# Optimization experiments

Measured on AMD Instinct MI355X. Metric: run time of the kernel, lower is better.

## Reference

```python
import jax, jax.numpy as jnp
import numpy as np

EPS = float(np.finfo(np.float32).eps)
NUM_SAMPLES = 2000
Y0 = 0.9999
BATCH, ACTION_DIM = 4096, 16


def setup_inputs() -> dict:
    key = jax.random.key(0)
    k1, k2, k3 = jax.random.split(key, 3)
    mean = jax.random.normal(k1, (BATCH, ACTION_DIM), dtype=jnp.float32)
    std = jax.random.uniform(k2, (BATCH, ACTION_DIM), dtype=jnp.float32)
    uniform = jax.random.uniform(k3, (BATCH, ACTION_DIM, 1), dtype=jnp.float32)
    return {"mean": mean, "std": std, "uniform": uniform}


def reference(mean, std, uniform):
    # Matches CustomDistribution.__init__ (std + eps) and rsample().
    std = std + EPS                                     # (B, A)
    grid = jnp.linspace(-Y0, Y0, NUM_SAMPLES, dtype=jnp.float32)  # (S,)
    x = grid[None, None, :]                             # broadcast to (1, 1, S)
    mu = mean[..., None]                                # (B, A, 1)
    sg = std[..., None]                                 # (B, A, 1)

    atanh_x = 0.5 * jnp.log((1.0 + x) / (1.0 - x) + EPS)
    log_term = (atanh_x - mu) ** 2 / (-2.0 * sg ** 2)
    # unnormalized density of tanh-Gaussian on the grid: (B, A, S)
    probs = (1.0 / (1.0 - x ** 2)) * (1.0 / jnp.sqrt(2.0 * jnp.pi * sg ** 2)) * jnp.exp(log_term)
    probs = probs / (probs.sum(axis=2, keepdims=True) + EPS)

    cdf = jnp.cumsum(probs, axis=2)                     # (B, A, S)
    # first index where uniform < cdf (argmax of bool picks first True)
    sample_idx = jnp.argmax(uniform < cdf, axis=2)      # (B, A) int

    sampled_values = grid[sample_idx]                   # (B, A)
    sampled_probs = jnp.take_along_axis(probs, sample_idx[..., None], axis=2)[..., 0]
    return sampled_values, sampled_probs
```

## Files before the change

kernel.cpp:

```cpp
#include <hip/hip_runtime.h>
#include <math.h>

#define NS 2000
#define NPAD 2048
#define EPS_F 1.1920928955078125e-07f
#define LOG2E 1.4426950408889634f
#define X0F  -0.9999f
#define HREC 999.64996f
#define HF   1.00040020e-3f
#define B8C  2.7842747f
#define SIGM 2.0e-3f
#define PCELL_MIN 1.0e-4f
#define FLIP_TOL 0.012f

__device__ __forceinline__ float exp2_hw(float x) {
    return __builtin_amdgcn_exp2f(x);
}

template <int CTRL, int RMASK>
static __device__ __forceinline__ float dpp_add(float x) {
    int t = __builtin_amdgcn_update_dpp(0, __float_as_int(x), CTRL, RMASK, 0xf, true);
    return x + __int_as_float(t);
}
static __device__ __forceinline__ float scan64(float x) {
    x = dpp_add<0x111, 0xf>(x);
    x = dpp_add<0x112, 0xf>(x);
    x = dpp_add<0x114, 0xf>(x);
    x = dpp_add<0x118, 0xf>(x);
    x = dpp_add<0x142, 0xa>(x);
    x = dpp_add<0x143, 0xc>(x);
    return x;
}
static __device__ __forceinline__ float scan32(float x) {
    x = dpp_add<0x111, 0xf>(x);
    x = dpp_add<0x112, 0xf>(x);
    x = dpp_add<0x114, 0xf>(x);
    x = dpp_add<0x118, 0xf>(x);
    x = dpp_add<0x142, 0xa>(x);
    return x;
}
static __device__ __forceinline__ float bcast_lane(float x, int lane_sgpr) {
    return __int_as_float(__builtin_amdgcn_readlane(__float_as_int(x), lane_sgpr));
}

static __device__ __forceinline__ float cdf01(float t) {
    float z = -t * 0.70710678f;
    float az = fabsf(z);
    float k = 1.0f / fmaf(0.3275911f, az, 1.0f);
    float poly = fmaf(k, 1.061405429f, -1.453152027f);
    poly = fmaf(k, poly, 1.421413741f);
    poly = fmaf(k, poly, -0.284496736f);
    poly = fmaf(k, poly, 0.254829592f);
    poly *= k;
    float e = exp2_hw(-az * az * LOG2E);
    float erfc_az = poly * e;
    float erfc_z = (z < 0.0f) ? (2.0f - erfc_az) : erfc_az;
    return 0.5f * erfc_z;
}
static __device__ __forceinline__ float erfinv_f(float x) {
    float w = -logf(fmaf(-x, x, 1.0f));
    bool c = w < 5.0f;
    float ww = c ? (w - 2.5f) : (sqrtf(w) - 3.0f);
    float p = c ? 2.81022636e-08f : -0.000200214257f;
    p = fmaf(p, ww, c ? 3.43273939e-07f : 0.000100950558f);
    p = fmaf(p, ww, c ? -3.5233877e-06f : 0.00134934322f);
    p = fmaf(p, ww, c ? -4.39150654e-06f : -0.00367342844f);
    p = fmaf(p, ww, c ? 0.00021858087f : 0.00573950773f);
    p = fmaf(p, ww, c ? -0.00125372503f : -0.0076224613f);
    p = fmaf(p, ww, c ? -0.00417768164f : 0.00943887047f);
    p = fmaf(p, ww, c ? 0.246640727f : 1.00167406f);
    p = fmaf(p, ww, c ? 1.50140941f : 2.83297682f);
    return p * x;
}
static __device__ __forceinline__ float cosh2f(float t) {
    float e = exp2_hw(2.8853901f * t);
    float re = __builtin_amdgcn_rcpf(e);
    return 0.25f * (e + 2.0f + re);
}

__global__ void build_table(float2* __restrict__ tabT, float2* __restrict__ tab2,
                            int* __restrict__ cnt) {
    int i = blockIdx.x * blockDim.x + threadIdx.x;
    if (i == 0) *cnt = 0;
    if (i >= NPAD) return;
    float a = 0.0f, lw = -1000.0f;
    if (i < NS) {
        const double y0 = -0.9999, y1 = 0.9999;
        const double step = (y1 - y0) / 1999.0;
        float x = (i == NS - 1) ? (float)y1 : (float)(y0 + (double)i * step);
        float ratio = (1.0f + x) / (1.0f - x) + EPS_F;
        a = 0.5f * logf(ratio);
        float w = 1.0f / (1.0f - x * x);
        lw = log2f(w);
    }
    tab2[i] = make_float2(a, lw);
    int l = i >> 5, k = i & 31, kk = k >> 1, h = k & 1;
    tabT[(kk * 64 + l) * 2 + h] = make_float2(a, lw);
}

__global__ __launch_bounds__(256) void analytic_kernel(
    const float* __restrict__ mean, const float* __restrict__ stdv,
    const float* __restrict__ uni, const float2* __restrict__ tab2,
    float* __restrict__ out_vals, float* __restrict__ out_probs,
    int* __restrict__ list, int* __restrict__ cnt, int nElem) {
    int gid = blockIdx.x * blockDim.x + threadIdx.x;
    if (gid >= nElem) return;

    const float mu = mean[gid];
    const float sg = stdv[gid] + EPS_F;
    const float u = uni[gid];
    const float inv_sg = 1.0f / sg;
    const float rd2 = -0.72134752f * inv_sg * inv_sg;
    const float nc = 0.39894228f * inv_sg;
    const float hn = HF * nc;

    float ql[8];
    float qlow = 0.0f, qhigh = 0.0f;
    #pragma unroll
    for (int c = 0; c < 8; c++) {
        float2 al = tab2[c];
        float d = al.x - mu;
        ql[c] = exp2_hw(fmaf(d * d, rd2, al.y));
        qlow += ql[c];
        float2 ah = tab2[NS - 8 + c];
        float dh = ah.x - mu;
        qhigh += exp2_hw(fmaf(dh * dh, rd2, ah.y));
    }

    const float PloB = cdf01((-B8C - mu) * inv_sg);
    const float PhiB = cdf01(( B8C - mu) * inv_sg);
    const float Qbulk = fmaxf(PhiB - PloB, 0.0f) / hn;
    const float Stot = qlow + Qbulk + qhigh;
    const float denomP = fmaf(nc, Stot, EPS_F);
    const float tt = u * denomP / nc;

    bool ok = (sg >= SIGM * cosh2f(fminf(fabsf(mu), B8C)));
    ok = ok && (tt < qlow + Qbulk);

    int idx = -1;
    float qsel = 0.0f;

    {
        float cum = 0.0f;
        #pragma unroll
        for (int c = 0; c < 8; c++) {
            cum += ql[c];
            if (idx < 0 && cum > tt) { idx = c; qsel = ql[c]; }
        }
    }
    if (ok && idx < 0) {
        float Pt = fmaf(tt - qlow, hn, PloB);
        float xx = fmaf(2.0f, Pt, -1.0f);
        xx = fminf(fmaxf(xx, -0.99999994f), 0.99999994f);
        float ts = 1.41421356f * erfinv_f(xx);
        float as = fmaf(sg, ts, mu);
        float e2 = exp2_hw(as * 2.8853901f);
        float tau = 1.0f - 2.0f / (e2 + 1.0f);
        float fi = fmaf(tau - X0F, HREC, -0.5f);
        int is = (int)floorf(fi) + 1;
        ok = ok && (is >= 8) && (is <= 1991)
                && (sg >= SIGM * cosh2f(fabsf(as)));
        is = min(max(is, 8), 1991);
        float2 al = tab2[is];
        float d = al.x - mu;
        float qi = exp2_hw(fmaf(d * d, rd2, al.y));
        float pn = nc * qi / denomP;
        ok = ok && (pn >= PCELL_MIN);
        float hl = HF * cosh2f(fabsf(as));
        float r = hl * inv_sg;
        float arg = r * (fabsf(as - mu) * inv_sg + 0.5f * r);
        float ratio = exp2_hw(LOG2E * fminf(arg, 20.0f)) - 1.0f;
        ok = ok && (pn * ratio <= FLIP_TOL);
        if (ok) { idx = is; qsel = qi; }
    }

    if (ok && idx >= 0) {
        const double y0 = -0.9999, y1 = 0.9999;
        const double step = (y1 - y0) / 1999.0;
        float gv = (idx == NS - 1) ? (float)y1 : (float)(y0 + (double)idx * step);
        out_vals[gid] = gv;
        out_probs[gid] = nc * qsel / denomP;
    } else {
        int slot = atomicAdd(cnt, 1);
        list[slot] = gid;
    }
}

__global__ __launch_bounds__(256) void fallback_kernel(
    const float* __restrict__ mean, const float* __restrict__ stdv,
    const float* __restrict__ uni, const float4* __restrict__ gT,
    const float4* __restrict__ gP,
    float* __restrict__ out_vals, float* __restrict__ out_probs,
    const int* __restrict__ list, const int* __restrict__ cnt) {
    const int count = *cnt;
    if (blockIdx.x * 4 >= count) return;

    __shared__ float4 sT[NPAD / 2];
    __shared__ float4 sPbuf[NPAD / 2];
    const float2* sP = (const float2*)sPbuf;
    for (int t = threadIdx.x; t < NPAD / 2; t += 256) {
        sT[t] = gT[t];
        sPbuf[t] = gP[t];
    }
    __syncthreads();

    const int lane = threadIdx.x & 63;
    const int wid = threadIdx.x >> 6;
    const int stride = gridDim.x << 2;

    for (int slot = blockIdx.x * 4 + wid; slot < count; slot += stride) {
        const int elem = list[slot];
        const float mu = mean[elem];
        const float sg = stdv[elem] + EPS_F;
        const float u = uni[elem];
        const float sg2 = sg * sg;
        const float rden2 = LOG2E / (-2.0f * sg2);
        const float normc = 1.0f / sqrtf(6.2831853071795864f * sg2);

        float s0 = 0.0f, s1 = 0.0f;
        #pragma unroll
        for (int kk = 0; kk < 16; kk++) {
            float4 v = sT[kk * 64 + lane];
            float d0 = v.x - mu;
            s0 += exp2_hw(fmaf(d0 * d0, rden2, v.y));
            float d1 = v.z - mu;
            s1 += exp2_hw(fmaf(d1 * d1, rden2, v.w));
        }
        float s = s0 + s1;

        float incl = scan64(s);
        const float S = bcast_lane(incl, 63);
        const float denom = S * normc + EPS_F;
        const float tt = (u * denom) / normc;

        unsigned long long mgt = __ballot(incl > tt);
        int jstar = mgt ? __builtin_ctzll(mgt) : 64;
        int jj = (jstar < 64) ? jstar : 0;
        float exclb = bcast_lane(incl - s, jj);

        int c = lane & 31;
        float2 al = sP[jj * 32 + c];
        float d = al.x - mu;
        float cum = scan32(exp2_hw(fmaf(d * d, rden2, al.y)));
        cum += exclb;
        unsigned int m2 = (unsigned int)(__ballot(cum > tt) & 0xffffffffULL);
        int sub = m2 ? (int)__builtin_ctz(m2) : 32;
        int idx = (jstar >= 64) ? 0 : min(jj * 32 + sub, NS - 1);

        if (lane == 0) {
            float2 al2 = sP[idx];
            float dd = al2.x - mu;
            float pk = exp2_hw(fmaf(dd * dd, rden2, al2.y)) * normc;
            const double y0 = -0.9999, y1 = 0.9999;
            const double step = (y1 - y0) / 1999.0;
            float gv = (idx == NS - 1) ? (float)y1
                                       : (float)(y0 + (double)idx * step);
            out_vals[elem] = gv;
            out_probs[elem] = pk / denom;
        }
    }
}

extern "C" void kernel_launch(void* const* d_in, const int* in_sizes, int n_in,
                              void* d_out, int out_size, void* d_ws, size_t ws_size,
                              hipStream_t stream) {
    const float* mean = (const float*)d_in[0];
    const float* stdv = (const float*)d_in[1];
    const float* uni = (const float*)d_in[2];
    float* out = (float*)d_out;
    const int nElem = in_sizes[0];
    float* out_vals = out;
    float* out_probs = out + nElem;

    char* ws = (char*)d_ws;
    float2* tabT = (float2*)ws;
    float2* tab2 = (float2*)(ws + 16384);
    int* cnt = (int*)(ws + 32768);
    int* list = (int*)(ws + 32768 + 16);

    build_table<<<NPAD / 256, 256, 0, stream>>>(tabT, tab2, cnt);

    analytic_kernel<<<(nElem + 255) / 256, 256, 0, stream>>>(
        mean, stdv, uni, tab2, out_vals, out_probs, list, cnt, nElem);

    fallback_kernel<<<2048, 256, 0, stream>>>(
        mean, stdv, uni, (const float4*)tabT, (const float4*)tab2,
        out_vals, out_probs, list, cnt);
}
```

Baseline: 75.65 us.

## Fuse table build, analytic sampling and fallback into one kernel

Replaces the three-kernel pipeline (table build, analytic fast path, global-list fallback) with a single kernel. Each block does the analytic path for its elements, collects failures in a shared-memory list, and only when that list is non-empty rebuilds the grid tables in LDS and runs the brute-force fallback for those elements. This removes two launches, the global atomic counter and list, and the global table round-trip. In exchange, table values are recomputed per element on the fast path (log/div per lookup), and every block with any fallback rebuilds the full table in LDS. Fallback work is also confined to its own block rather than spread across 2048 blocks.

```diff
diff --git a/kernel.cpp b/kernel.cpp
--- a/kernel.cpp
+++ b/kernel.cpp
@@ -12,6 +12,7 @@
 #define SIGM 2.0e-3f
 #define PCELL_MIN 1.0e-4f
 #define FLIP_TOL 0.012f
+#define BLOCK 256
 
 __device__ __forceinline__ float exp2_hw(float x) {
     return __builtin_amdgcn_exp2f(x);
@@ -78,138 +79,135 @@
     return 0.25f * (e + 2.0f + re);
 }
 
-__global__ void build_table(float2* __restrict__ tabT, float2* __restrict__ tab2,
-                            int* __restrict__ cnt) {
-    int i = blockIdx.x * blockDim.x + threadIdx.x;
-    if (i == 0) *cnt = 0;
-    if (i >= NPAD) return;
-    float a = 0.0f, lw = -1000.0f;
-    if (i < NS) {
-        const double y0 = -0.9999, y1 = 0.9999;
-        const double step = (y1 - y0) / 1999.0;
-        float x = (i == NS - 1) ? (float)y1 : (float)(y0 + (double)i * step);
-        float ratio = (1.0f + x) / (1.0f - x) + EPS_F;
-        a = 0.5f * logf(ratio);
-        float w = 1.0f / (1.0f - x * x);
-        lw = log2f(w);
-    }
-    tab2[i] = make_float2(a, lw);
-    int l = i >> 5, k = i & 31, kk = k >> 1, h = k & 1;
-    tabT[(kk * 64 + l) * 2 + h] = make_float2(a, lw);
-}
-
-__global__ __launch_bounds__(256) void analytic_kernel(
+static __device__ __forceinline__ float2 cellAL(int i) {
+    const double y0 = -0.9999, y1 = 0.9999;
+    const double step = (y1 - y0) / 1999.0;
+    float x = (i == NS - 1) ? (float)y1 : (float)(y0 + (double)i * step);
+    float ratio = (1.0f + x) / (1.0f - x) + EPS_F;
+    float a = 0.5f * logf(ratio);
+    float lw = log2f(1.0f / (1.0f - x * x));
+    return make_float2(a, lw);
+}
+
+__global__ __launch_bounds__(BLOCK) void fused_kernel(
     const float* __restrict__ mean, const float* __restrict__ stdv,
-    const float* __restrict__ uni, const float2* __restrict__ tab2,
-    float* __restrict__ out_vals, float* __restrict__ out_probs,
-    int* __restrict__ list, int* __restrict__ cnt, int nElem) {
-    int gid = blockIdx.x * blockDim.x + threadIdx.x;
-    if (gid >= nElem) return;
-
-    const float mu = mean[gid];
-    const float sg = stdv[gid] + EPS_F;
-    const float u = uni[gid];
-    const float inv_sg = 1.0f / sg;
-    const float rd2 = -0.72134752f * inv_sg * inv_sg;
-    const float nc = 0.39894228f * inv_sg;
-    const float hn = HF * nc;
-
-    float ql[8];
-    float qlow = 0.0f, qhigh = 0.0f;
-    #pragma unroll
-    for (int c = 0; c < 8; c++) {
-        float2 al = tab2[c];
-        float d = al.x - mu;
-        ql[c] = exp2_hw(fmaf(d * d, rd2, al.y));
-        qlow += ql[c];
-        float2 ah = tab2[NS - 8 + c];
-        float dh = ah.x - mu;
-        qhigh += exp2_hw(fmaf(dh * dh, rd2, ah.y));
-    }
-
-    const float PloB = cdf01((-B8C - mu) * inv_sg);
-    const float PhiB = cdf01(( B8C - mu) * inv_sg);
-    const float Qbulk = fmaxf(PhiB - PloB, 0.0f) / hn;
-    const float Stot = qlow + Qbulk + qhigh;
-    const float denomP = fmaf(nc, Stot, EPS_F);
-    const float tt = u * denomP / nc;
-
-    bool ok = (sg >= SIGM * cosh2f(fminf(fabsf(mu), B8C)));
-    ok = ok && (tt < qlow + Qbulk);
-
-    int idx = -1;
-    float qsel = 0.0f;
-
-    {
-        float cum = 0.0f;
+    const float* __restrict__ uni,
+    float* __restrict__ out_vals, float* __restrict__ out_probs, int nElem) {
+
+    __shared__ float4 sT[NPAD / 2];
+    __shared__ float4 sPb[NPAD / 2];
+    __shared__ int fbList[BLOCK];
+    __shared__ int fbCnt;
+
+    const int tid = threadIdx.x;
+    if (tid == 0) fbCnt = 0;
+    __syncthreads();
+
+    const int gid = blockIdx.x * BLOCK + tid;
+    if (gid < nElem) {
+        const float mu = mean[gid];
+        const float sg = stdv[gid] + EPS_F;
+        const float u = uni[gid];
+        const float inv_sg = 1.0f / sg;
+        const float rd2 = -0.72134752f * inv_sg * inv_sg;
+        const float nc = 0.39894228f * inv_sg;
+        const float hn = HF * nc;
+
+        float ql[8];
+        float qlow = 0.0f, qhigh = 0.0f;
         #pragma unroll
         for (int c = 0; c < 8; c++) {
-            cum += ql[c];
-            if (idx < 0 && cum > tt) { idx = c; qsel = ql[c]; }
-        }
-    }
-    if (ok && idx < 0) {
-        float Pt = fmaf(tt - qlow, hn, PloB);
-        float xx = fmaf(2.0f, Pt, -1.0f);
-        xx = fminf(fmaxf(xx, -0.99999994f), 0.99999994f);
-        float ts = 1.41421356f * erfinv_f(xx);
-        float as = fmaf(sg, ts, mu);
-        float e2 = exp2_hw(as * 2.8853901f);
-        float tau = 1.0f - 2.0f / (e2 + 1.0f);
-        float fi = fmaf(tau - X0F, HREC, -0.5f);
-        int is = (int)floorf(fi) + 1;
-        ok = ok && (is >= 8) && (is <= 1991)
-                && (sg >= SIGM * cosh2f(fabsf(as)));
-        is = min(max(is, 8), 1991);
-        float2 al = tab2[is];
-        float d = al.x - mu;
-        float qi = exp2_hw(fmaf(d * d, rd2, al.y));
-        float pn = nc * qi / denomP;
-        ok = ok && (pn >= PCELL_MIN);
-        float hl = HF * cosh2f(fabsf(as));
-        float r = hl * inv_sg;
-        float arg = r * (fabsf(as - mu) * inv_sg + 0.5f * r);
-        float ratio = exp2_hw(LOG2E * fminf(arg, 20.0f)) - 1.0f;
-        ok = ok && (pn * ratio <= FLIP_TOL);
-        if (ok) { idx = is; qsel = qi; }
-    }
-
-    if (ok && idx >= 0) {
-        const double y0 = -0.9999, y1 = 0.9999;
-        const double step = (y1 - y0) / 1999.0;
-        float gv = (idx == NS - 1) ? (float)y1 : (float)(y0 + (double)idx * step);
-        out_vals[gid] = gv;
-        out_probs[gid] = nc * qsel / denomP;
-    } else {
-        int slot = atomicAdd(cnt, 1);
-        list[slot] = gid;
-    }
-}
-
-__global__ __launch_bounds__(256) void fallback_kernel(
-    const float* __restrict__ mean, const float* __restrict__ stdv,
-    const float* __restrict__ uni, const float4* __restrict__ gT,
-    const float4* __restrict__ gP,
-    float* __restrict__ out_vals, float* __restrict__ out_probs,
-    const int* __restrict__ list, const int* __restrict__ cnt) {
-    const int count = *cnt;
-    if (blockIdx.x * 4 >= count) return;
-
-    __shared__ float4 sT[NPAD / 2];
-    __shared__ float4 sPbuf[NPAD / 2];
-    const float2* sP = (const float2*)sPbuf;
-    for (int t = threadIdx.x; t < NPAD / 2; t += 256) {
-        sT[t] = gT[t];
-        sPbuf[t] = gP[t];
+            float2 al = cellAL(c);
+            float d = al.x - mu;
+            ql[c] = exp2_hw(fmaf(d * d, rd2, al.y));
+            qlow += ql[c];
+            float2 ah = cellAL(NS - 8 + c);
+            float dh = ah.x - mu;
+            qhigh += exp2_hw(fmaf(dh * dh, rd2, ah.y));
+        }
+
+        const float PloB = cdf01((-B8C - mu) * inv_sg);
+        const float PhiB = cdf01(( B8C - mu) * inv_sg);
+        const float Qbulk = fmaxf(PhiB - PloB, 0.0f) / hn;
+        const float Stot = qlow + Qbulk + qhigh;
+        const float denomP = fmaf(nc, Stot, EPS_F);
+        const float tt = u * denomP / nc;
+
+        bool ok = (sg >= SIGM * cosh2f(fminf(fabsf(mu), B8C)));
+        ok = ok && (tt < qlow + Qbulk);
+
+        int idx = -1;
+        float qsel = 0.0f;
+
+        {
+            float cum = 0.0f;
+            #pragma unroll
+            for (int c = 0; c < 8; c++) {
+                cum += ql[c];
+                if (idx < 0 && cum > tt) { idx = c; qsel = ql[c]; }
+            }
+        }
+        if (ok && idx < 0) {
+            float Pt = fmaf(tt - qlow, hn, PloB);
+            float xx = fmaf(2.0f, Pt, -1.0f);
+            xx = fminf(fmaxf(xx, -0.99999994f), 0.99999994f);
+            float ts = 1.41421356f * erfinv_f(xx);
+            float as = fmaf(sg, ts, mu);
+            float e2 = exp2_hw(as * 2.8853901f);
+            float tau = 1.0f - 2.0f / (e2 + 1.0f);
+            float fi = fmaf(tau - X0F, HREC, -0.5f);
+            int is = (int)floorf(fi) + 1;
+            ok = ok && (is >= 8) && (is <= 1991)
+                    && (sg >= SIGM * cosh2f(fabsf(as)));
+            is = min(max(is, 8), 1991);
+            float2 al = cellAL(is);
+            float d = al.x - mu;
+            float qi = exp2_hw(fmaf(d * d, rd2, al.y));
+            float pn = nc * qi / denomP;
+            ok = ok && (pn >= PCELL_MIN);
+            float hl = HF * cosh2f(fabsf(as));
+            float r = hl * inv_sg;
+            float arg = r * (fabsf(as - mu) * inv_sg + 0.5f * r);
+            float ratio = exp2_hw(LOG2E * fminf(arg, 20.0f)) - 1.0f;
+            ok = ok && (pn * ratio <= FLIP_TOL);
+            if (ok) { idx = is; qsel = qi; }
+        }
+
+        if (ok && idx >= 0) {
+            const double y0 = -0.9999, y1 = 0.9999;
+            const double step = (y1 - y0) / 1999.0;
+            float gv = (idx == NS - 1) ? (float)y1
+                                       : (float)(y0 + (double)idx * step);
+            out_vals[gid] = gv;
+            out_probs[gid] = nc * qsel / denomP;
+        } else {
+            int s = atomicAdd(&fbCnt, 1);
+            fbList[s] = tid;
+        }
     }
     __syncthreads();
-
-    const int lane = threadIdx.x & 63;
-    const int wid = threadIdx.x >> 6;
-    const int stride = gridDim.x << 2;
-
-    for (int slot = blockIdx.x * 4 + wid; slot < count; slot += stride) {
-        const int elem = list[slot];
+    const int cnt = fbCnt;
+    if (cnt == 0) return;
+
+    {
+        float2* sP2 = (float2*)sPb;
+        float2* sT2 = (float2*)sT;
+        #pragma unroll
+        for (int r = 0; r < 8; r++) {
+            int i = tid * 8 + r;
+            float2 alw = (i < NS) ? cellAL(i) : make_float2(0.0f, -1000.0f);
+            sP2[i] = alw;
+            int l = i >> 5, k = i & 31, kk = k >> 1, h = k & 1;
+            sT2[(kk * 64 + l) * 2 + h] = alw;
+        }
+    }
+    __syncthreads();
+
+    const float2* sP = (const float2*)sPb;
+    const int lane = tid & 63;
+    const int wid = tid >> 6;
+    for (int slot = wid; slot < cnt; slot += 4) {
+        const int elem = blockIdx.x * BLOCK + fbList[slot];
         const float mu = mean[elem];
         const float sg = stdv[elem] + EPS_F;
         const float u = uni[elem];
@@ -271,19 +269,9 @@
     const int nElem = in_sizes[0];
     float* out_vals = out;
     float* out_probs = out + nElem;
-
-    char* ws = (char*)d_ws;
-    float2* tabT = (float2*)ws;
-    float2* tab2 = (float2*)(ws + 16384);
-    int* cnt = (int*)(ws + 32768);
-    int* list = (int*)(ws + 32768 + 16);
-
-    build_table<<<NPAD / 256, 256, 0, stream>>>(tabT, tab2, cnt);
-
-    analytic_kernel<<<(nElem + 255) / 256, 256, 0, stream>>>(
-        mean, stdv, uni, tab2, out_vals, out_probs, list, cnt, nElem);
-
-    fallback_kernel<<<2048, 256, 0, stream>>>(
-        mean, stdv, uni, (const float4*)tabT, (const float4*)tab2,
-        out_vals, out_probs, list, cnt);
-}
+    (void)d_ws; (void)ws_size;
+
+    const int grid = (nElem + BLOCK - 1) / BLOCK;
+    fused_kernel<<<grid, BLOCK, 0, stream>>>(mean, stdv, uni,
+                                             out_vals, out_probs, nElem);
+}
```

Result: faster. 63.16 us (-16.5%).
